# Performance work log

Hardware: AMD Instinct MI355X
Metric: run time of the kernel (lower is better)

## Reference

```python
import jax, jax.numpy as jnp
import numpy as np

INPUT_SIZE = 1
HIDDEN_SIZE = 50
OUTPUT_SIZE = 1
BATCH = 16384
SEQ_LEN = 2048


def setup_inputs() -> dict:
    key = jax.random.key(0)
    ks = jax.random.split(key, 8)
    s_ih = 1.0 / np.sqrt(HIDDEN_SIZE)
    x = jax.random.normal(ks[0], (BATCH, SEQ_LEN, INPUT_SIZE), dtype=jnp.float32)
    # PyTorch nn.LSTM params: weight_ih_l0 [4H, I], weight_hh_l0 [4H, H], biases [4H]
    w_ih = jax.random.uniform(ks[1], (4 * HIDDEN_SIZE, INPUT_SIZE), jnp.float32, -s_ih, s_ih)
    w_hh = jax.random.uniform(ks[2], (4 * HIDDEN_SIZE, HIDDEN_SIZE), jnp.float32, -s_ih, s_ih)
    b_ih = jax.random.uniform(ks[3], (4 * HIDDEN_SIZE,), jnp.float32, -s_ih, s_ih)
    b_hh = jax.random.uniform(ks[4], (4 * HIDDEN_SIZE,), jnp.float32, -s_ih, s_ih)
    # fc head: Linear(hidden_size, output_size)
    w_fc = jax.random.uniform(ks[5], (OUTPUT_SIZE, HIDDEN_SIZE), jnp.float32, -s_ih, s_ih)
    b_fc = jax.random.uniform(ks[6], (OUTPUT_SIZE,), jnp.float32, -s_ih, s_ih)
    return {"x": x, "w_ih": w_ih, "w_hh": w_hh, "b_ih": b_ih, "b_hh": b_hh,
            "w_fc": w_fc, "b_fc": b_fc}


def reference(x, w_ih, w_hh, b_ih, b_hh, w_fc, b_fc):
    B = x.shape[0]
    H = w_hh.shape[1]
    xT = jnp.swapaxes(x, 0, 1)                      # [T, B, I]
    # precompute input contribution to gates for all timesteps: [T, B, 4H]
    x_proj = jnp.einsum('tbi,gi->tbg', xT, w_ih) + b_ih + b_hh

    def step(carry, xp):
        h, c = carry
        gates = xp + h @ w_hh.T                     # [B, 4H]
        i, f, g, o = jnp.split(gates, 4, axis=-1)   # PyTorch gate order: i, f, g, o
        i = jax.nn.sigmoid(i)
        f = jax.nn.sigmoid(f)
        g = jnp.tanh(g)
        o = jax.nn.sigmoid(o)
        c = f * c + i * g
        h = o * jnp.tanh(c)
        return (h, c), None

    h0 = jnp.zeros((B, H), x.dtype)
    (h_last, _), _ = jax.lax.scan(step, (h0, h0), x_proj)
    # fc applied to last timestep's hidden state
    return h_last @ w_fc.T + b_fc                   # [B, 1]
```

## Files before the change

### kernel.cpp

```cpp
#include <hip/hip_runtime.h>
#include <cstdint>

typedef __attribute__((ext_vector_type(8))) short short8;
typedef __attribute__((ext_vector_type(4))) float f32x4;
typedef __attribute__((ext_vector_type(2))) float f32x2;

#define TPB  256
#define MB   16
#define HS   50
#define HSTR 72
#define XSTR 68
#define L2E  1.4426950408889634f
#define L2E2 2.8853900817779268f

__device__ __forceinline__ float ex2(float x) {
#if __has_builtin(__builtin_amdgcn_exp2f)
  return __builtin_amdgcn_exp2f(x);
#else
  float r; asm("v_exp_f32 %0, %1" : "=v"(r) : "v"(x)); return r;
#endif
}
__device__ __forceinline__ float rcp_(float x) {
#if __has_builtin(__builtin_amdgcn_rcpf)
  return __builtin_amdgcn_rcpf(x);
#else
  float r; asm("v_rcp_f32 %0, %1" : "=v"(r) : "v"(x)); return r;
#endif
}
__device__ __forceinline__ unsigned short bf16_rne(float f) {
  unsigned r;
  asm("v_cvt_pk_bf16_f32 %0, %1, %2" : "=v"(r) : "v"(f), "v"(f));
  return (unsigned short)r;
}
__device__ __forceinline__ unsigned cvtpk2(float a, float b) {
  unsigned r;
  asm("v_cvt_pk_bf16_f32 %0, %1, %2" : "=v"(r) : "v"(a), "v"(b));
  return r;
}
__device__ __forceinline__ float bf16f(unsigned short h) {
  union { unsigned u; float f; } v; v.u = ((unsigned)h) << 16; return v.f;
}
__device__ __forceinline__ unsigned packx(float f) {
  unsigned short hi = bf16_rne(f);
  unsigned short lo = bf16_rne(f - bf16f(hi));
  return (unsigned)hi | ((unsigned)lo << 16);
}
__device__ __forceinline__ int swcol(int row, int col) {
  return (((col >> 3) ^ ((row >> 2) & 3)) << 3) | (col & 7);
}

__global__ __launch_bounds__(TPB, 4)
void lstm_mfma10(const float* __restrict__ x,
                 const float* __restrict__ w_ih,
                 const float* __restrict__ w_hh,
                 const float* __restrict__ b_ih,
                 const float* __restrict__ b_hh,
                 const float* __restrict__ w_fc,
                 const float* __restrict__ b_fc,
                 float* __restrict__ out, int T)
{
  __shared__ __attribute__((aligned(16))) unsigned short hbuf[2][MB][HSTR];
  __shared__ __attribute__((aligned(16))) unsigned x_lds[2][MB][XSTR];

  const int tid  = threadIdx.x;
  const int wid  = tid >> 6;
  const int lane = tid & 63;
  const int l15  = lane & 15;
  const int lhi  = lane >> 4;
  const int b0   = blockIdx.x * MB;
  const int rho  = (blockIdx.x >> 8) & 3;
  const int g    = (wid + rho) & 3;
  const int j    = g * 16 + l15;
  const bool jval  = (j < HS);
  const bool light = (g == 3);
  const bool inj   = (lhi == 2);

  short8 Wh[4][2];
  #pragma unroll
  for (int s = 0; s < 4; ++s) {
    const float sc = (s == 2) ? L2E2 : L2E;
    float wsc = 0.f, bsc = 0.f;
    if (jval) {
      int row = s * HS + j;
      wsc = w_ih[row] * sc;
      bsc = (b_ih[row] + b_hh[row]) * sc;
    }
    const unsigned short wh = bf16_rne(wsc);
    const unsigned short wl = bf16_rne(wsc - bf16f(wh));
    const unsigned short bh = bf16_rne(bsc);
    const unsigned short bl = bf16_rne(bsc - bf16f(bh));
    #pragma unroll
    for (int i = 0; i < 8; ++i) {
      int k = lhi * 8 + i;
      Wh[s][0][i] = (short)(jval ? bf16_rne(w_hh[(s * HS + j) * HS + k] * sc) : 0);
    }
    #pragma unroll
    for (int i = 0; i < 8; ++i) {
      int k = 32 + lhi * 8 + i;
      unsigned short hv = 0;
      if (jval) {
        if (k < HS)                  hv = bf16_rne(w_hh[(s * HS + j) * HS + k] * sc);
        else if (k == 50 || k == 51) hv = wh;
        else if (k == 52)            hv = wl;
        else if (k == 53)            hv = bh;
        else if (k == 54)            hv = bl;
      }
      Wh[s][1][i] = (short)hv;
    }
  }

  for (int idx = tid; idx < 2 * MB * HSTR; idx += TPB)
    (&hbuf[0][0][0])[idx] = 0;
  {
    int bb = tid >> 4, tt = (tid & 15) * 4;
    const f32x4 v = *(const f32x4*)(x + (size_t)(b0 + bb) * T + tt);
    uint4 up;
    up.x = packx(v[0]); up.y = packx(v[1]); up.z = packx(v[2]); up.w = packx(v[3]);
    *(uint4*)&x_lds[0][bb][tt] = up;
  }
  __syncthreads();

  const int keyr  = (l15 >> 2) & 3;
  const int offA0 = l15 * HSTR + ((lhi ^ keyr) << 3);
  const int offA1 = l15 * HSTR + (((lhi + 4) ^ keyr) << 3);
  const int offW  = l15 * HSTR + ((((g * 2 + (lhi >> 1)) ^ keyr) << 3)) + (lhi & 1) * 4;

  f32x2 cA = {0.f, 0.f}, cB = {0.f, 0.f};
  f32x4 xf = {0.f, 0.f, 0.f, 0.f};
  const int nch = T >> 6;

  auto ELEM = [&](f32x2 ai, f32x2 af, f32x2 ag, f32x2 ao, f32x2& c2) -> f32x2 {
    f32x2 u, v, w, z, q, rD, r3, vm1;
    u[0] = ex2(-ai[0]); u[1] = ex2(-ai[1]);
    v[0] = ex2( ag[0]); v[1] = ex2( ag[1]);
    w[0] = ex2(-af[0]); w[1] = ex2(-af[1]);
    z[0] = ex2(-ao[0]); z[1] = ex2(-ao[1]);
    f32x2 t1 = (u + 1.f) * (v + 1.f);
    f32x2 wp = w + 1.f;
    f32x2 D  = t1 * wp;
    rD[0] = rcp_(D[0]); rD[1] = rcp_(D[1]);
    vm1[0] = fmaf(v[0], L2E2, -L2E2);
    vm1[1] = fmaf(v[1], L2E2, -L2E2);
    f32x2 num = c2 * t1 + vm1 * wp;
    f32x2 cn = num * rD;
    cn[0] = fminf(fmaxf(cn[0], -86.f), 86.f);
    cn[1] = fminf(fmaxf(cn[1], -86.f), 86.f);
    c2 = cn;
    q[0] = ex2(cn[0]); q[1] = ex2(cn[1]);
    f32x2 t3 = (z + 1.f) * (q + 1.f);
    r3[0] = rcp_(t3[0]); r3[1] = rcp_(t3[1]);
    return (q - 1.f) * r3;
  };

  auto STEP = [&](const unsigned short* hr, unsigned short* hw,
                  const unsigned* xrow, int slot) {
    const unsigned xp = xrow[slot];
    const short8 B0 = *(const short8*)(hr + offA0);
    union { short8 s8; unsigned u[4]; } b1;
    b1.s8 = *(const short8*)(hr + offA1);
    b1.u[1] = inj ? xp : b1.u[1];
    b1.u[2] = inj ? ((xp & 0xFFFFu) | 0x3F800000u) : b1.u[2];
    b1.u[3] = inj ? 0x00003F80u : b1.u[3];

    __builtin_amdgcn_s_setprio(1);
    f32x4 acc[4];
    #pragma unroll
    for (int s = 0; s < 4; ++s) {
      acc[s] = __builtin_amdgcn_mfma_f32_16x16x32_bf16(Wh[s][0], B0,
                   (f32x4){0.f, 0.f, 0.f, 0.f}, 0, 0, 0);
      acc[s] = __builtin_amdgcn_mfma_f32_16x16x32_bf16(Wh[s][1], b1.s8, acc[s], 0, 0, 0);
    }
    __builtin_amdgcn_s_setprio(0);

    f32x2 h2A = ELEM((f32x2){acc[0][0], acc[0][1]}, (f32x2){acc[1][0], acc[1][1]},
                     (f32x2){acc[2][0], acc[2][1]}, (f32x2){acc[3][0], acc[3][1]}, cA);
    unsigned hx = cvtpk2(h2A[0], h2A[1]);
    if (!light) {
      f32x2 h2B = ELEM((f32x2){acc[0][2], acc[0][3]}, (f32x2){acc[1][2], acc[1][3]},
                       (f32x2){acc[2][2], acc[2][3]}, (f32x2){acc[3][2], acc[3][3]}, cB);
      uint2 hwv;
      hwv.x = hx;
      hwv.y = cvtpk2(h2B[0], h2B[1]);
      *(uint2*)(hw + offW) = hwv;
    } else {
      *(unsigned*)(hw + offW) = hx;
    }

    __syncthreads();
  };

  unsigned short* hb0 = &hbuf[0][0][0];
  unsigned short* hb1 = &hbuf[1][0][0];

  for (int ch = 0; ch < nch; ++ch) {
    const int par = ch & 1;
    const unsigned* xrow = &x_lds[par][l15][0];
    int slot = 0;
    #pragma unroll 1
    for (int i = 0; i < 8; ++i) {
      STEP(hb0, hb1, xrow, slot); STEP(hb1, hb0, xrow, slot + 1); slot += 2;
    }
    if (ch + 1 < nch)
      xf = *(const f32x4*)(x + (size_t)(b0 + (tid >> 4)) * T + (ch + 1) * 64 + (tid & 15) * 4);
    #pragma unroll 1
    for (int i = 0; i < 14; ++i) {
      STEP(hb0, hb1, xrow, slot); STEP(hb1, hb0, xrow, slot + 1); slot += 2;
    }
    if (ch + 1 < nch) {
      uint4 up;
      up.x = packx(xf[0]); up.y = packx(xf[1]);
      up.z = packx(xf[2]); up.w = packx(xf[3]);
      *(uint4*)&x_lds[par ^ 1][tid >> 4][(tid & 15) * 4] = up;
    }
    #pragma unroll 1
    for (int i = 0; i < 10; ++i) {
      STEP(hb0, hb1, xrow, slot); STEP(hb1, hb0, xrow, slot + 1); slot += 2;
    }
  }

  if (tid < MB) {
    const unsigned short* hfin = hb0 + tid * HSTR;
    float s = 0.f;
    for (int jj = 0; jj < HS; ++jj)
      s = fmaf(bf16f(hfin[swcol(tid, jj)]), w_fc[jj], s);
    out[b0 + tid] = s + b_fc[0];
  }
}

extern "C" void kernel_launch(void* const* d_in, const int* in_sizes, int n_in,
                              void* d_out, int out_size, void* d_ws, size_t ws_size,
                              hipStream_t stream) {
  const float* x    = (const float*)d_in[0];
  const float* w_ih = (const float*)d_in[1];
  const float* w_hh = (const float*)d_in[2];
  const float* b_ih = (const float*)d_in[3];
  const float* b_hh = (const float*)d_in[4];
  const float* w_fc = (const float*)d_in[5];
  const float* b_fc = (const float*)d_in[6];
  float* out = (float*)d_out;

  const int B = out_size;
  const int T = in_sizes[0] / B;

  dim3 grid(B / MB), block(TPB);
  hipLaunchKernelGGL(lstm_mfma10, grid, block, 0, stream,
                     x, w_ih, w_hh, b_ih, b_hh, w_fc, b_fc, out, T);
}
```

Baseline: 1.930 ms.

## Process two 16-row batch groups per block to amortize barriers and weight registers

Each block now handles 32 batch rows as two independent 16-row MFMA groups. The same in-register W_hh fragments are reused for both groups, and the per-timestep __syncthreads cost is spread over twice the work. The interleaved MFMAs and elementwise chains also give more independent instructions to hide latency within a wave. In exchange, register pressure and LDS use roughly double, so launch bounds drop to 2 blocks per CU, the grid is halved, and the wave-to-gate rotation rho now also depends on blockIdx parity.

```diff
diff --git a/kernel.cpp b/kernel.cpp
--- a/kernel.cpp
+++ b/kernel.cpp
@@ -6,7 +6,7 @@
 typedef __attribute__((ext_vector_type(2))) float f32x2;
 
 #define TPB  256
-#define MB   16
+#define MB   32
 #define HS   50
 #define HSTR 72
 #define XSTR 68
@@ -49,8 +49,8 @@
   return (((col >> 3) ^ ((row >> 2) & 3)) << 3) | (col & 7);
 }
 
-__global__ __launch_bounds__(TPB, 4)
-void lstm_mfma10(const float* __restrict__ x,
+__global__ __launch_bounds__(TPB, 2)
+void lstm_mfma11(const float* __restrict__ x,
                  const float* __restrict__ w_ih,
                  const float* __restrict__ w_hh,
                  const float* __restrict__ b_ih,
@@ -68,7 +68,7 @@
   const int l15  = lane & 15;
   const int lhi  = lane >> 4;
   const int b0   = blockIdx.x * MB;
-  const int rho  = (blockIdx.x >> 8) & 3;
+  const int rho  = (blockIdx.x + (blockIdx.x >> 8)) & 3;
   const int g    = (wid + rho) & 3;
   const int j    = g * 16 + l15;
   const bool jval  = (j < HS);
@@ -112,11 +112,15 @@
   for (int idx = tid; idx < 2 * MB * HSTR; idx += TPB)
     (&hbuf[0][0][0])[idx] = 0;
   {
-    int bb = tid >> 4, tt = (tid & 15) * 4;
-    const f32x4 v = *(const f32x4*)(x + (size_t)(b0 + bb) * T + tt);
-    uint4 up;
-    up.x = packx(v[0]); up.y = packx(v[1]); up.z = packx(v[2]); up.w = packx(v[3]);
-    *(uint4*)&x_lds[0][bb][tt] = up;
+    int bb = tid >> 3, base = (tid & 7) * 8;
+    const float* xr = x + (size_t)(b0 + bb) * T + base;
+    const f32x4 v0 = *(const f32x4*)(xr);
+    const f32x4 v1 = *(const f32x4*)(xr + 4);
+    uint4 u0, u1;
+    u0.x = packx(v0[0]); u0.y = packx(v0[1]); u0.z = packx(v0[2]); u0.w = packx(v0[3]);
+    u1.x = packx(v1[0]); u1.y = packx(v1[1]); u1.z = packx(v1[2]); u1.w = packx(v1[3]);
+    *(uint4*)&x_lds[0][bb][base]     = u0;
+    *(uint4*)&x_lds[0][bb][base + 4] = u1;
   }
   __syncthreads();
 
@@ -124,9 +128,11 @@
   const int offA0 = l15 * HSTR + ((lhi ^ keyr) << 3);
   const int offA1 = l15 * HSTR + (((lhi + 4) ^ keyr) << 3);
   const int offW  = l15 * HSTR + ((((g * 2 + (lhi >> 1)) ^ keyr) << 3)) + (lhi & 1) * 4;
-
-  f32x2 cA = {0.f, 0.f}, cB = {0.f, 0.f};
-  f32x4 xf = {0.f, 0.f, 0.f, 0.f};
+  const int GRP   = 16 * HSTR;
+
+  f32x2 cA0 = {0.f, 0.f}, cB0 = {0.f, 0.f};
+  f32x2 cA1 = {0.f, 0.f}, cB1 = {0.f, 0.f};
+  f32x4 xf0 = {0.f, 0.f, 0.f, 0.f}, xf1 = {0.f, 0.f, 0.f, 0.f};
   const int nch = T >> 6;
 
   auto ELEM = [&](f32x2 ai, f32x2 af, f32x2 ag, f32x2 ao, f32x2& c2) -> f32x2 {
@@ -153,37 +159,60 @@
   };
 
   auto STEP = [&](const unsigned short* hr, unsigned short* hw,
-                  const unsigned* xrow, int slot) {
-    const unsigned xp = xrow[slot];
-    const short8 B0 = *(const short8*)(hr + offA0);
-    union { short8 s8; unsigned u[4]; } b1;
-    b1.s8 = *(const short8*)(hr + offA1);
-    b1.u[1] = inj ? xp : b1.u[1];
-    b1.u[2] = inj ? ((xp & 0xFFFFu) | 0x3F800000u) : b1.u[2];
-    b1.u[3] = inj ? 0x00003F80u : b1.u[3];
+                  const unsigned* xrowA, const unsigned* xrowB, int slot) {
+    const unsigned xpa = xrowA[slot];
+    const unsigned xpb = xrowB[slot];
+
+    const short8 B0a = *(const short8*)(hr + offA0);
+    union { short8 s8; unsigned u[4]; } b1a, b1b;
+    b1a.s8 = *(const short8*)(hr + offA1);
+    b1a.u[1] = inj ? xpa : b1a.u[1];
+    b1a.u[2] = inj ? ((xpa & 0xFFFFu) | 0x3F800000u) : b1a.u[2];
+    b1a.u[3] = inj ? 0x00003F80u : b1a.u[3];
+    const short8 B0b = *(const short8*)(hr + offA0 + GRP);
+    b1b.s8 = *(const short8*)(hr + offA1 + GRP);
+    b1b.u[1] = inj ? xpb : b1b.u[1];
+    b1b.u[2] = inj ? ((xpb & 0xFFFFu) | 0x3F800000u) : b1b.u[2];
+    b1b.u[3] = inj ? 0x00003F80u : b1b.u[3];
 
     __builtin_amdgcn_s_setprio(1);
-    f32x4 acc[4];
+    f32x4 acc0[4], acc1[4];
     #pragma unroll
     for (int s = 0; s < 4; ++s) {
-      acc[s] = __builtin_amdgcn_mfma_f32_16x16x32_bf16(Wh[s][0], B0,
-                   (f32x4){0.f, 0.f, 0.f, 0.f}, 0, 0, 0);
-      acc[s] = __builtin_amdgcn_mfma_f32_16x16x32_bf16(Wh[s][1], b1.s8, acc[s], 0, 0, 0);
+      acc0[s] = __builtin_amdgcn_mfma_f32_16x16x32_bf16(Wh[s][0], B0a,
+                    (f32x4){0.f, 0.f, 0.f, 0.f}, 0, 0, 0);
+      acc1[s] = __builtin_amdgcn_mfma_f32_16x16x32_bf16(Wh[s][0], B0b,
+                    (f32x4){0.f, 0.f, 0.f, 0.f}, 0, 0, 0);
+      acc0[s] = __builtin_amdgcn_mfma_f32_16x16x32_bf16(Wh[s][1], b1a.s8, acc0[s], 0, 0, 0);
+      acc1[s] = __builtin_amdgcn_mfma_f32_16x16x32_bf16(Wh[s][1], b1b.s8, acc1[s], 0, 0, 0);
     }
     __builtin_amdgcn_s_setprio(0);
 
-    f32x2 h2A = ELEM((f32x2){acc[0][0], acc[0][1]}, (f32x2){acc[1][0], acc[1][1]},
-                     (f32x2){acc[2][0], acc[2][1]}, (f32x2){acc[3][0], acc[3][1]}, cA);
-    unsigned hx = cvtpk2(h2A[0], h2A[1]);
-    if (!light) {
-      f32x2 h2B = ELEM((f32x2){acc[0][2], acc[0][3]}, (f32x2){acc[1][2], acc[1][3]},
-                       (f32x2){acc[2][2], acc[2][3]}, (f32x2){acc[3][2], acc[3][3]}, cB);
-      uint2 hwv;
-      hwv.x = hx;
-      hwv.y = cvtpk2(h2B[0], h2B[1]);
-      *(uint2*)(hw + offW) = hwv;
-    } else {
-      *(unsigned*)(hw + offW) = hx;
+    {
+      f32x2 h2A = ELEM((f32x2){acc0[0][0], acc0[0][1]}, (f32x2){acc0[1][0], acc0[1][1]},
+                       (f32x2){acc0[2][0], acc0[2][1]}, (f32x2){acc0[3][0], acc0[3][1]}, cA0);
+      unsigned hx = cvtpk2(h2A[0], h2A[1]);
+      if (!light) {
+        f32x2 h2B = ELEM((f32x2){acc0[0][2], acc0[0][3]}, (f32x2){acc0[1][2], acc0[1][3]},
+                         (f32x2){acc0[2][2], acc0[2][3]}, (f32x2){acc0[3][2], acc0[3][3]}, cB0);
+        uint2 hwv; hwv.x = hx; hwv.y = cvtpk2(h2B[0], h2B[1]);
+        *(uint2*)(hw + offW) = hwv;
+      } else {
+        *(unsigned*)(hw + offW) = hx;
+      }
+    }
+    {
+      f32x2 h2A = ELEM((f32x2){acc1[0][0], acc1[0][1]}, (f32x2){acc1[1][0], acc1[1][1]},
+                       (f32x2){acc1[2][0], acc1[2][1]}, (f32x2){acc1[3][0], acc1[3][1]}, cA1);
+      unsigned hx = cvtpk2(h2A[0], h2A[1]);
+      if (!light) {
+        f32x2 h2B = ELEM((f32x2){acc1[0][2], acc1[0][3]}, (f32x2){acc1[1][2], acc1[1][3]},
+                         (f32x2){acc1[2][2], acc1[2][3]}, (f32x2){acc1[3][2], acc1[3][3]}, cB1);
+        uint2 hwv; hwv.x = hx; hwv.y = cvtpk2(h2B[0], h2B[1]);
+        *(uint2*)(hw + offW + GRP) = hwv;
+      } else {
+        *(unsigned*)(hw + offW + GRP) = hx;
+      }
     }
 
     __syncthreads();
@@ -194,27 +223,36 @@
 
   for (int ch = 0; ch < nch; ++ch) {
     const int par = ch & 1;
-    const unsigned* xrow = &x_lds[par][l15][0];
+    const unsigned* xrowA = &x_lds[par][l15][0];
+    const unsigned* xrowB = &x_lds[par][l15 + 16][0];
     int slot = 0;
     #pragma unroll 1
     for (int i = 0; i < 8; ++i) {
-      STEP(hb0, hb1, xrow, slot); STEP(hb1, hb0, xrow, slot + 1); slot += 2;
-    }
-    if (ch + 1 < nch)
-      xf = *(const f32x4*)(x + (size_t)(b0 + (tid >> 4)) * T + (ch + 1) * 64 + (tid & 15) * 4);
+      STEP(hb0, hb1, xrowA, xrowB, slot);
+      STEP(hb1, hb0, xrowA, xrowB, slot + 1); slot += 2;
+    }
+    if (ch + 1 < nch) {
+      const float* xr = x + (size_t)(b0 + (tid >> 3)) * T + (ch + 1) * 64 + (tid & 7) * 8;
+      xf0 = *(const f32x4*)(xr);
+      xf1 = *(const f32x4*)(xr + 4);
+    }
     #pragma unroll 1
     for (int i = 0; i < 14; ++i) {
-      STEP(hb0, hb1, xrow, slot); STEP(hb1, hb0, xrow, slot + 1); slot += 2;
+      STEP(hb0, hb1, xrowA, xrowB, slot);
+      STEP(hb1, hb0, xrowA, xrowB, slot + 1); slot += 2;
     }
     if (ch + 1 < nch) {
-      uint4 up;
-      up.x = packx(xf[0]); up.y = packx(xf[1]);
-      up.z = packx(xf[2]); up.w = packx(xf[3]);
-      *(uint4*)&x_lds[par ^ 1][tid >> 4][(tid & 15) * 4] = up;
+      uint4 u0, u1;
+      u0.x = packx(xf0[0]); u0.y = packx(xf0[1]); u0.z = packx(xf0[2]); u0.w = packx(xf0[3]);
+      u1.x = packx(xf1[0]); u1.y = packx(xf1[1]); u1.z = packx(xf1[2]); u1.w = packx(xf1[3]);
+      int bb = tid >> 3, base = (tid & 7) * 8;
+      *(uint4*)&x_lds[par ^ 1][bb][base]     = u0;
+      *(uint4*)&x_lds[par ^ 1][bb][base + 4] = u1;
     }
     #pragma unroll 1
     for (int i = 0; i < 10; ++i) {
-      STEP(hb0, hb1, xrow, slot); STEP(hb1, hb0, xrow, slot + 1); slot += 2;
+      STEP(hb0, hb1, xrowA, xrowB, slot);
+      STEP(hb1, hb0, xrowA, xrowB, slot + 1); slot += 2;
     }
   }
 
@@ -243,6 +281,6 @@
   const int T = in_sizes[0] / B;
 
   dim3 grid(B / MB), block(TPB);
-  hipLaunchKernelGGL(lstm_mfma10, grid, block, 0, stream,
+  hipLaunchKernelGGL(lstm_mfma11, grid, block, 0, stream,
                      x, w_ih, w_hh, b_ih, b_hh, w_fc, b_fc, out, T);
 }
```

Result: slower. 2.051 ms (+6.3%).

## Run each LSTM tile in one wavefront to drop per-step block barriers

Applied to the files above, without the earlier changes.

The four-wave block, where each wave computed one gate group and a __syncthreads followed every timestep, becomes a single 64-lane wavefront that computes all four gate groups itself. The h state now uses one in-place LDS buffer instead of a double buffer. The x and bias injection is written directly into the h tile rather than patched into registers. This removes the per-timestep barrier and the cross-wave handoff. In exchange each wave holds four times the weight registers and runs 32 MFMAs plus seven ELEM blocks back to back per step. It also leaves only one wave per SIMD, so almost no other waves are available to hide latency.

```diff
diff --git a/kernel.cpp b/kernel.cpp
--- a/kernel.cpp
+++ b/kernel.cpp
@@ -5,7 +5,7 @@
 typedef __attribute__((ext_vector_type(4))) float f32x4;
 typedef __attribute__((ext_vector_type(2))) float f32x2;
 
-#define TPB  256
+#define TPB  64
 #define MB   16
 #define HS   50
 #define HSTR 72
@@ -49,84 +49,90 @@
   return (((col >> 3) ^ ((row >> 2) & 3)) << 3) | (col & 7);
 }
 
-__global__ __launch_bounds__(TPB, 4)
-void lstm_mfma10(const float* __restrict__ x,
-                 const float* __restrict__ w_ih,
-                 const float* __restrict__ w_hh,
-                 const float* __restrict__ b_ih,
-                 const float* __restrict__ b_hh,
-                 const float* __restrict__ w_fc,
-                 const float* __restrict__ b_fc,
-                 float* __restrict__ out, int T)
+__global__ __launch_bounds__(TPB, 1)
+void lstm_solo(const float* __restrict__ x,
+               const float* __restrict__ w_ih,
+               const float* __restrict__ w_hh,
+               const float* __restrict__ b_ih,
+               const float* __restrict__ b_hh,
+               const float* __restrict__ w_fc,
+               const float* __restrict__ b_fc,
+               float* __restrict__ out, int T)
 {
-  __shared__ __attribute__((aligned(16))) unsigned short hbuf[2][MB][HSTR];
+  __shared__ __attribute__((aligned(16))) unsigned short h_lds[MB][HSTR];
   __shared__ __attribute__((aligned(16))) unsigned x_lds[2][MB][XSTR];
 
-  const int tid  = threadIdx.x;
-  const int wid  = tid >> 6;
-  const int lane = tid & 63;
+  const int lane = threadIdx.x;
   const int l15  = lane & 15;
   const int lhi  = lane >> 4;
   const int b0   = blockIdx.x * MB;
-  const int rho  = (blockIdx.x >> 8) & 3;
-  const int g    = (wid + rho) & 3;
-  const int j    = g * 16 + l15;
-  const bool jval  = (j < HS);
-  const bool light = (g == 3);
-  const bool inj   = (lhi == 2);
-
-  short8 Wh[4][2];
+
+  short8 Wh[4][4][2];
   #pragma unroll
-  for (int s = 0; s < 4; ++s) {
-    const float sc = (s == 2) ? L2E2 : L2E;
-    float wsc = 0.f, bsc = 0.f;
-    if (jval) {
-      int row = s * HS + j;
-      wsc = w_ih[row] * sc;
-      bsc = (b_ih[row] + b_hh[row]) * sc;
-    }
-    const unsigned short wh = bf16_rne(wsc);
-    const unsigned short wl = bf16_rne(wsc - bf16f(wh));
-    const unsigned short bh = bf16_rne(bsc);
-    const unsigned short bl = bf16_rne(bsc - bf16f(bh));
+  for (int g = 0; g < 4; ++g) {
+    const int j = g * 16 + l15;
+    const bool jv = (j < HS);
     #pragma unroll
-    for (int i = 0; i < 8; ++i) {
-      int k = lhi * 8 + i;
-      Wh[s][0][i] = (short)(jval ? bf16_rne(w_hh[(s * HS + j) * HS + k] * sc) : 0);
-    }
-    #pragma unroll
-    for (int i = 0; i < 8; ++i) {
-      int k = 32 + lhi * 8 + i;
-      unsigned short hv = 0;
-      if (jval) {
-        if (k < HS)                  hv = bf16_rne(w_hh[(s * HS + j) * HS + k] * sc);
-        else if (k == 50 || k == 51) hv = wh;
-        else if (k == 52)            hv = wl;
-        else if (k == 53)            hv = bh;
-        else if (k == 54)            hv = bl;
-      }
-      Wh[s][1][i] = (short)hv;
-    }
-  }
-
-  for (int idx = tid; idx < 2 * MB * HSTR; idx += TPB)
-    (&hbuf[0][0][0])[idx] = 0;
-  {
-    int bb = tid >> 4, tt = (tid & 15) * 4;
-    const f32x4 v = *(const f32x4*)(x + (size_t)(b0 + bb) * T + tt);
-    uint4 up;
-    up.x = packx(v[0]); up.y = packx(v[1]); up.z = packx(v[2]); up.w = packx(v[3]);
-    *(uint4*)&x_lds[0][bb][tt] = up;
-  }
-  __syncthreads();
+    for (int s = 0; s < 4; ++s) {
+      const float sc = (s == 2) ? L2E2 : L2E;
+      float wsc = 0.f, bsc = 0.f;
+      if (jv) {
+        int row = s * HS + j;
+        wsc = w_ih[row] * sc;
+        bsc = (b_ih[row] + b_hh[row]) * sc;
+      }
+      const unsigned short wh = bf16_rne(wsc);
+      const unsigned short wl = bf16_rne(wsc - bf16f(wh));
+      const unsigned short bh = bf16_rne(bsc);
+      const unsigned short bl = bf16_rne(bsc - bf16f(bh));
+      #pragma unroll
+      for (int i = 0; i < 8; ++i) {
+        int k = lhi * 8 + i;
+        Wh[g][s][0][i] = (short)(jv ? bf16_rne(w_hh[(s * HS + j) * HS + k] * sc) : 0);
+      }
+      #pragma unroll
+      for (int i = 0; i < 8; ++i) {
+        int k = 32 + lhi * 8 + i;
+        unsigned short hv = 0;
+        if (jv) {
+          if (k < HS)                  hv = bf16_rne(w_hh[(s * HS + j) * HS + k] * sc);
+          else if (k == 50 || k == 51) hv = wh;
+          else if (k == 52)            hv = wl;
+          else if (k == 53)            hv = bh;
+          else if (k == 54)            hv = bl;
+        }
+        Wh[g][s][1][i] = (short)hv;
+      }
+    }
+  }
+
+  unsigned short* hs = &h_lds[0][0];
+
+  for (int idx = lane; idx < MB * HSTR; idx += TPB) hs[idx] = 0;
 
   const int keyr  = (l15 >> 2) & 3;
   const int offA0 = l15 * HSTR + ((lhi ^ keyr) << 3);
   const int offA1 = l15 * HSTR + (((lhi + 4) ^ keyr) << 3);
-  const int offW  = l15 * HSTR + ((((g * 2 + (lhi >> 1)) ^ keyr) << 3)) + (lhi & 1) * 4;
-
-  f32x2 cA = {0.f, 0.f}, cB = {0.f, 0.f};
-  f32x4 xf = {0.f, 0.f, 0.f, 0.f};
+  const int offX  = l15 * HSTR + ((6 ^ keyr) << 3);
+
+  if (lane < 16)
+    hs[offX + 6] = 0x3F80;
+
+  {
+    const int bb = lane >> 2, base = (lane & 3) * 16;
+    const float* xr = x + (size_t)(b0 + bb) * T + base;
+    #pragma unroll
+    for (int q = 0; q < 4; ++q) {
+      const f32x4 v = *(const f32x4*)(xr + q * 4);
+      uint4 up;
+      up.x = packx(v[0]); up.y = packx(v[1]); up.z = packx(v[2]); up.w = packx(v[3]);
+      *(uint4*)&x_lds[0][bb][base + q * 4] = up;
+    }
+  }
+
+  f32x2 cA[4] = {{0.f,0.f},{0.f,0.f},{0.f,0.f},{0.f,0.f}};
+  f32x2 cB[3] = {{0.f,0.f},{0.f,0.f},{0.f,0.f}};
+  f32x4 xf0 = {0,0,0,0}, xf1 = {0,0,0,0}, xf2 = {0,0,0,0}, xf3 = {0,0,0,0};
   const int nch = T >> 6;
 
   auto ELEM = [&](f32x2 ai, f32x2 af, f32x2 ag, f32x2 ao, f32x2& c2) -> f32x2 {
@@ -152,78 +158,85 @@
     return (q - 1.f) * r3;
   };
 
-  auto STEP = [&](const unsigned short* hr, unsigned short* hw,
-                  const unsigned* xrow, int slot) {
-    const unsigned xp = xrow[slot];
-    const short8 B0 = *(const short8*)(hr + offA0);
-    union { short8 s8; unsigned u[4]; } b1;
-    b1.s8 = *(const short8*)(hr + offA1);
-    b1.u[1] = inj ? xp : b1.u[1];
-    b1.u[2] = inj ? ((xp & 0xFFFFu) | 0x3F800000u) : b1.u[2];
-    b1.u[3] = inj ? 0x00003F80u : b1.u[3];
-
-    __builtin_amdgcn_s_setprio(1);
-    f32x4 acc[4];
+  auto STEP = [&](const unsigned* xrow, int slot) {
+    if (lane < 16) {
+      const unsigned xp = xrow[slot];
+      *(unsigned*)(hs + offX + 2) = xp;
+      *(unsigned*)(hs + offX + 4) = (xp & 0xFFFFu) | 0x3F800000u;
+    }
+    const short8 B0 = *(const short8*)(hs + offA0);
+    const short8 B1 = *(const short8*)(hs + offA1);
+
     #pragma unroll
-    for (int s = 0; s < 4; ++s) {
-      acc[s] = __builtin_amdgcn_mfma_f32_16x16x32_bf16(Wh[s][0], B0,
-                   (f32x4){0.f, 0.f, 0.f, 0.f}, 0, 0, 0);
-      acc[s] = __builtin_amdgcn_mfma_f32_16x16x32_bf16(Wh[s][1], b1.s8, acc[s], 0, 0, 0);
-    }
-    __builtin_amdgcn_s_setprio(0);
-
-    f32x2 h2A = ELEM((f32x2){acc[0][0], acc[0][1]}, (f32x2){acc[1][0], acc[1][1]},
-                     (f32x2){acc[2][0], acc[2][1]}, (f32x2){acc[3][0], acc[3][1]}, cA);
-    unsigned hx = cvtpk2(h2A[0], h2A[1]);
-    if (!light) {
-      f32x2 h2B = ELEM((f32x2){acc[0][2], acc[0][3]}, (f32x2){acc[1][2], acc[1][3]},
-                       (f32x2){acc[2][2], acc[2][3]}, (f32x2){acc[3][2], acc[3][3]}, cB);
-      uint2 hwv;
-      hwv.x = hx;
-      hwv.y = cvtpk2(h2B[0], h2B[1]);
-      *(uint2*)(hw + offW) = hwv;
-    } else {
-      *(unsigned*)(hw + offW) = hx;
-    }
-
-    __syncthreads();
+    for (int g = 0; g < 4; ++g) {
+      f32x4 a0 = __builtin_amdgcn_mfma_f32_16x16x32_bf16(Wh[g][0][0], B0,
+                     (f32x4){0.f,0.f,0.f,0.f}, 0, 0, 0);
+      f32x4 a1 = __builtin_amdgcn_mfma_f32_16x16x32_bf16(Wh[g][1][0], B0,
+                     (f32x4){0.f,0.f,0.f,0.f}, 0, 0, 0);
+      f32x4 a2 = __builtin_amdgcn_mfma_f32_16x16x32_bf16(Wh[g][2][0], B0,
+                     (f32x4){0.f,0.f,0.f,0.f}, 0, 0, 0);
+      f32x4 a3 = __builtin_amdgcn_mfma_f32_16x16x32_bf16(Wh[g][3][0], B0,
+                     (f32x4){0.f,0.f,0.f,0.f}, 0, 0, 0);
+      a0 = __builtin_amdgcn_mfma_f32_16x16x32_bf16(Wh[g][0][1], B1, a0, 0, 0, 0);
+      a1 = __builtin_amdgcn_mfma_f32_16x16x32_bf16(Wh[g][1][1], B1, a1, 0, 0, 0);
+      a2 = __builtin_amdgcn_mfma_f32_16x16x32_bf16(Wh[g][2][1], B1, a2, 0, 0, 0);
+      a3 = __builtin_amdgcn_mfma_f32_16x16x32_bf16(Wh[g][3][1], B1, a3, 0, 0, 0);
+
+      const int offW = l15 * HSTR +
+          ((((g * 2 + (lhi >> 1)) ^ keyr) << 3)) + (lhi & 1) * 4;
+
+      f32x2 hA = ELEM((f32x2){a0[0], a0[1]}, (f32x2){a1[0], a1[1]},
+                      (f32x2){a2[0], a2[1]}, (f32x2){a3[0], a3[1]}, cA[g]);
+      if (g < 3) {
+        f32x2 hB = ELEM((f32x2){a0[2], a0[3]}, (f32x2){a1[2], a1[3]},
+                        (f32x2){a2[2], a2[3]}, (f32x2){a3[2], a3[3]}, cB[g]);
+        uint2 hwv;
+        hwv.x = cvtpk2(hA[0], hA[1]);
+        hwv.y = cvtpk2(hB[0], hB[1]);
+        *(uint2*)(hs + offW) = hwv;
+      } else {
+        if (lhi == 0)
+          *(unsigned*)(hs + offW) = cvtpk2(hA[0], hA[1]);
+      }
+    }
   };
 
-  unsigned short* hb0 = &hbuf[0][0][0];
-  unsigned short* hb1 = &hbuf[1][0][0];
-
   for (int ch = 0; ch < nch; ++ch) {
-    const int par = ch & 1;
-    const unsigned* xrow = &x_lds[par][l15][0];
+    const unsigned* xrow = &x_lds[ch & 1][l15][0];
     int slot = 0;
     #pragma unroll 1
-    for (int i = 0; i < 8; ++i) {
-      STEP(hb0, hb1, xrow, slot); STEP(hb1, hb0, xrow, slot + 1); slot += 2;
-    }
-    if (ch + 1 < nch)
-      xf = *(const f32x4*)(x + (size_t)(b0 + (tid >> 4)) * T + (ch + 1) * 64 + (tid & 15) * 4);
+    for (int i = 0; i < 16; ++i) STEP(xrow, slot++);
+    if (ch + 1 < nch) {
+      const float* xr = x + (size_t)(b0 + (lane >> 2)) * T + (ch + 1) * 64 + (lane & 3) * 16;
+      xf0 = *(const f32x4*)(xr);
+      xf1 = *(const f32x4*)(xr + 4);
+      xf2 = *(const f32x4*)(xr + 8);
+      xf3 = *(const f32x4*)(xr + 12);
+    }
     #pragma unroll 1
-    for (int i = 0; i < 14; ++i) {
-      STEP(hb0, hb1, xrow, slot); STEP(hb1, hb0, xrow, slot + 1); slot += 2;
-    }
+    for (int i = 0; i < 28; ++i) STEP(xrow, slot++);
     if (ch + 1 < nch) {
-      uint4 up;
-      up.x = packx(xf[0]); up.y = packx(xf[1]);
-      up.z = packx(xf[2]); up.w = packx(xf[3]);
-      *(uint4*)&x_lds[par ^ 1][tid >> 4][(tid & 15) * 4] = up;
+      const int bb = lane >> 2, base = (lane & 3) * 16;
+      uint4 u0, u1, u2, u3;
+      u0.x = packx(xf0[0]); u0.y = packx(xf0[1]); u0.z = packx(xf0[2]); u0.w = packx(xf0[3]);
+      u1.x = packx(xf1[0]); u1.y = packx(xf1[1]); u1.z = packx(xf1[2]); u1.w = packx(xf1[3]);
+      u2.x = packx(xf2[0]); u2.y = packx(xf2[1]); u2.z = packx(xf2[2]); u2.w = packx(xf2[3]);
+      u3.x = packx(xf3[0]); u3.y = packx(xf3[1]); u3.z = packx(xf3[2]); u3.w = packx(xf3[3]);
+      unsigned* dst = &x_lds[(ch + 1) & 1][bb][base];
+      *(uint4*)(dst)      = u0;
+      *(uint4*)(dst + 4)  = u1;
+      *(uint4*)(dst + 8)  = u2;
+      *(uint4*)(dst + 12) = u3;
     }
     #pragma unroll 1
-    for (int i = 0; i < 10; ++i) {
-      STEP(hb0, hb1, xrow, slot); STEP(hb1, hb0, xrow, slot + 1); slot += 2;
-    }
-  }
-
-  if (tid < MB) {
-    const unsigned short* hfin = hb0 + tid * HSTR;
+    for (int i = 0; i < 20; ++i) STEP(xrow, slot++);
+  }
+
+  if (lane < 16) {
     float s = 0.f;
     for (int jj = 0; jj < HS; ++jj)
-      s = fmaf(bf16f(hfin[swcol(tid, jj)]), w_fc[jj], s);
-    out[b0 + tid] = s + b_fc[0];
+      s = fmaf(bf16f(hs[lane * HSTR + swcol(lane, jj)]), w_fc[jj], s);
+    out[b0 + lane] = s + b_fc[0];
   }
 }
 
@@ -243,6 +256,6 @@
   const int T = in_sizes[0] / B;
 
   dim3 grid(B / MB), block(TPB);
-  hipLaunchKernelGGL(lstm_mfma10, grid, block, 0, stream,
+  hipLaunchKernelGGL(lstm_solo, grid, block, 0, stream,
                      x, w_ih, w_hh, b_ih, b_hh, w_fc, b_fc, out, T);
 }
```

After: 2.112 ms. +9.5%, slower.
